# Kernel optimization log

Hardware: AMD Instinct MI355X
Metric: run time of the kernel (lower is better)

The kernel has to match this reference:

```python
import jax, jax.numpy as jnp
import numpy as np
import math

B, S, D, H = 2, 2048, 1024, 16
HD = D // H  # head dim = 64


def setup_inputs() -> dict:
    key = jax.random.key(0)
    k1, k2, k3, k4, k5 = jax.random.split(key, 5)
    query = jax.random.normal(k1, (B, S, D), dtype=jnp.float32)
    # tail padding: sequence lengths 1536 and 1792 -> positions >= length are padded (True)
    lengths = jnp.array([1536, 1792], dtype=jnp.int32)
    padding_mask = jnp.arange(S, dtype=jnp.int32)[None, :] >= lengths[:, None]  # [B,S] bool
    qkv_w = jax.random.normal(k2, (3 * D, D), dtype=jnp.float32) * 0.02
    qkv_b = jax.random.uniform(k3, (3 * D,), dtype=jnp.float32, minval=-0.03, maxval=0.03)
    out_w = jax.random.normal(k4, (D, D), dtype=jnp.float32) * 0.02
    out_b = jax.random.uniform(k5, (D,), dtype=jnp.float32, minval=-0.03, maxval=0.03)
    return {"query": query, "padding_mask": padding_mask,
            "qkv_w": qkv_w, "qkv_b": qkv_b, "out_w": out_w, "out_b": out_b}


def reference(query, padding_mask, qkv_w, qkv_b, out_w, out_b):
    # self-attention path (qkv_same=True): fused qkv projection then split
    qkv = query @ qkv_w.T + qkv_b                      # [B,S,3D]
    q, k, v = jnp.split(qkv, 3, axis=-1)               # each [B,S,D]

    def split_heads(x):
        return x.reshape(B, S, H, HD).transpose(0, 2, 1, 3)  # [B,H,S,HD]

    q, k, v = split_heads(q), split_heads(k), split_heads(v)

    # scores scaled by sqrt(head_dim)
    w = jnp.einsum('bhqd,bhkd->bhqk', q, k) / math.sqrt(HD)  # [B,H,S,S]

    # causal (future) mask: strict upper triangle masked
    future = jnp.triu(jnp.ones((S, S), dtype=bool), 1)
    w = jnp.where(future[None, None, :, :], -jnp.inf, w)
    # key padding mask
    w = jnp.where(padding_mask[:, None, None, :], -jnp.inf, w)

    a = jax.nn.softmax(w, axis=-1)
    # rows of fully-padded sequences are zeroed (dropout is identity in eval)
    all_masked = jnp.all(padding_mask, axis=-1)        # [B]
    a = jnp.where(all_masked[:, None, None, None], 0.0, a)

    x = jnp.einsum('bhqk,bhkd->bhqd', a, v)            # [B,H,S,HD]
    x = x.transpose(0, 2, 1, 3).reshape(B, S, D)       # merge heads
    return x @ out_w.T + out_b
```

## Files before the change

### kernel.cpp

```cpp
#include <hip/hip_runtime.h>
#include <hip/hip_bf16.h>
#include <stdint.h>

#define S_  2048
#define B_  2
#define H_  16
#define D_  1024
#define HD_ 64

typedef short short8 __attribute__((ext_vector_type(8)));
typedef float f32x4  __attribute__((ext_vector_type(4)));
typedef float f32x16 __attribute__((ext_vector_type(16)));

__device__ __forceinline__ unsigned short bf16_rne(float f) {
  unsigned int u = __float_as_uint(f);
  u += 0x7fffu + ((u >> 16) & 1u);
  return (unsigned short)(u >> 16);
}

__device__ __forceinline__ f32x4 mfma_bf16(short8 a, short8 b, f32x4 c) {
  return __builtin_amdgcn_mfma_f32_16x16x32_bf16(a, b, c, 0, 0, 0);
}

__device__ __forceinline__ f32x16 mfma32(short8 a, short8 b, f32x16 c) {
  return __builtin_amdgcn_mfma_f32_32x32x16_bf16(a, b, c, 0, 0, 0);
}

__device__ __forceinline__ unsigned int cvtpk_bf16(float lo, float hi) {
  unsigned int r;
  asm("v_cvt_pk_bf16_f32 %0, %1, %2" : "=v"(r) : "v"(lo), "v"(hi));
  return r;
}

__global__ void cvt3_kernel(const float* __restrict__ a, unsigned short* __restrict__ oa, int na8,
                            const float* __restrict__ b, unsigned short* __restrict__ ob, int nb8,
                            const float* __restrict__ c, unsigned short* __restrict__ oc, int nc8) {
  int i = blockIdx.x * blockDim.x + threadIdx.x;
  const float* in; unsigned short* out; int idx;
  if (i < na8) { in = a; out = oa; idx = i; }
  else if (i < na8 + nb8) { in = b; out = ob; idx = i - na8; }
  else if (i < na8 + nb8 + nc8) { in = c; out = oc; idx = i - na8 - nb8; }
  else return;
  const float4* p = (const float4*)in + (size_t)idx * 2;
  float4 x = p[0], y = p[1];
  union { unsigned short u[8]; short8 v; } r;
  r.u[0] = bf16_rne(x.x); r.u[1] = bf16_rne(x.y);
  r.u[2] = bf16_rne(x.z); r.u[3] = bf16_rne(x.w);
  r.u[4] = bf16_rne(y.x); r.u[5] = bf16_rne(y.y);
  r.u[6] = bf16_rne(y.z); r.u[7] = bf16_rne(y.w);
  *((short8*)out + idx) = r.v;
}

__global__ void lengths_kernel(const void* __restrict__ mask, int* __restrict__ lens) {
  __shared__ int mn[B_];
  __shared__ int anyb;
  int t = threadIdx.x;
  if (t < B_) mn[t] = S_;
  if (t == 0) anyb = 0;
  __syncthreads();
  const unsigned char* mb = (const unsigned char*)mask;
  for (int i = t; i < B_ * S_; i += 256) {
    if (mb[i]) { anyb = 1; atomicMin(&mn[i >> 11], i & (S_ - 1)); }
  }
  __syncthreads();
  if (!anyb) {
    const int* mi = (const int*)mask;
    for (int i = t; i < B_ * S_; i += 256) {
      if (mi[i]) atomicMin(&mn[i >> 11], i & (S_ - 1));
    }
    __syncthreads();
  }
  if (t < B_) lens[t] = mn[t];
}

__global__ __launch_bounds__(512, 2) void gemm8p_kernel(
    const unsigned short* __restrict__ A,
    const unsigned short* __restrict__ W,
    int K, int NBX,
    const float* __restrict__ bias,
    unsigned short* __restrict__ qb,
    unsigned short* __restrict__ kb,
    unsigned short* __restrict__ vb) {
  __shared__ __align__(16) unsigned short lds[65536];

  const int nwg = gridDim.x;
  const int cpx = nwg >> 3;
  const int bid = blockIdx.x;
  const int virt = (bid & 7) * cpx + (bid >> 3);
  const int bx = virt % NBX, by = virt / NBX;
  const int tile_m = by * 256, tile_n = bx * 256;
  const int t = threadIdx.x;
  const int lane = t & 63, w = t >> 6;
  const int wm = w >> 2, wn = w & 3;
  const int l15 = lane & 15, lk = lane >> 4;
  const int NT = K >> 6;

  f32x4 acc[8][4];
#pragma unroll
  for (int i = 0; i < 8; i++)
#pragma unroll
    for (int j = 0; j < 4; j++) { f32x4 z = {0.f, 0.f, 0.f, 0.f}; acc[i][j] = z; }

  const int L0 = t, L1 = 512 + t;
  const int r0 = L0 >> 3, c0 = (L0 & 7) ^ (r0 & 7);
  const int r1 = L1 >> 3, c1 = (L1 & 7) ^ (r1 & 7);

#define STAGE_HALF(SRC, GROW0, DSTE, KC)                                      \
  {                                                                           \
    __builtin_amdgcn_global_load_lds(                                         \
        (const __attribute__((address_space(1))) void*)(                      \
            (SRC) + (size_t)((GROW0) + r0) * K + (KC) + c0 * 8),              \
        (__attribute__((address_space(3))) void*)(&lds[(DSTE) + L0 * 8]),     \
        16, 0, 0);                                                            \
    __builtin_amdgcn_global_load_lds(                                         \
        (const __attribute__((address_space(1))) void*)(                      \
            (SRC) + (size_t)((GROW0) + r1) * K + (KC) + c1 * 8),              \
        (__attribute__((address_space(3))) void*)(&lds[(DSTE) + L1 * 8]),     \
        16, 0, 0);                                                            \
  }

  STAGE_HALF(A, tile_m,        0,    0);
  STAGE_HALF(W, tile_n,        32768, 0);
  STAGE_HALF(A, tile_m + 128,  8192, 0);
  STAGE_HALF(W, tile_n + 128,  32768 + 8192, 0);
  asm volatile("s_waitcnt vmcnt(4)" ::: "memory");
  __builtin_amdgcn_s_barrier();

  for (int tc = 0; tc < NT; ++tc) {
    const int cb = (tc & 1) * 16384;
    const int ob = ((tc & 1) ^ 1) * 16384;
    int tn = tc + 1; if (tn >= NT) tn = NT - 1;
    const int k0n = tn << 6;

#pragma unroll
    for (int p = 0; p < 4; ++p) {
      const int mh = (p & 1);
      const int nh = (p >> 1);
      short8 af[4][2], bfr[2][2];
#pragma unroll
      for (int fi = 0; fi < 4; ++fi) {
        const int rl = fi * 32 + wm * 16 + l15;
#pragma unroll
        for (int ks = 0; ks < 2; ++ks) {
          const int sw = (ks * 4 + lk) ^ (rl & 7);
          af[fi][ks] = *(const short8*)&lds[cb + mh * 8192 + rl * 64 + sw * 8];
        }
      }
#pragma unroll
      for (int fj = 0; fj < 2; ++fj) {
        const int cl = wn * 32 + fj * 16 + l15;
#pragma unroll
        for (int ks = 0; ks < 2; ++ks) {
          const int sw = (ks * 4 + lk) ^ (cl & 7);
          bfr[fj][ks] =
              *(const short8*)&lds[32768 + cb + nh * 8192 + cl * 64 + sw * 8];
        }
      }
      if (p == 0)      STAGE_HALF(A, tile_m,       ob,                k0n)
      else if (p == 1) STAGE_HALF(W, tile_n,       32768 + ob,        k0n)
      else if (p == 2) STAGE_HALF(A, tile_m + 128, ob + 8192,         k0n)
      else             STAGE_HALF(W, tile_n + 128, 32768 + ob + 8192, k0n);
      if (p != 2) asm volatile("s_waitcnt vmcnt(4)" ::: "memory");
      else        asm volatile("" ::: "memory");
      __builtin_amdgcn_s_barrier();
      asm volatile("s_waitcnt lgkmcnt(0)" ::: "memory");
      __builtin_amdgcn_s_setprio(1);
#pragma unroll
      for (int fi = 0; fi < 4; ++fi)
#pragma unroll
        for (int fj = 0; fj < 2; ++fj)
#pragma unroll
          for (int ks = 0; ks < 2; ++ks)
            acc[mh * 4 + fi][nh * 2 + fj] =
                mfma_bf16(af[fi][ks], bfr[fj][ks], acc[mh * 4 + fi][nh * 2 + fj]);
      __builtin_amdgcn_s_setprio(0);
      __builtin_amdgcn_s_barrier();
    }
  }
  asm volatile("s_waitcnt vmcnt(0)" ::: "memory");
#undef STAGE_HALF

#pragma unroll
  for (int j = 0; j < 4; ++j) {
    const int gn = tile_n + (j >> 1) * 128 + wn * 32 + (j & 1) * 16 + l15;
    const float bv = bias[gn];
    const int which = gn >> 10, dd = gn & (D_ - 1);
    const int h = dd >> 6, d = dd & 63;
    unsigned short* dstp = (which == 0) ? qb : (which == 1) ? kb : vb;
    const float mul = (which == 0) ? 0.125f : 1.0f;
#pragma unroll
    for (int i = 0; i < 8; ++i) {
      const int gmb = tile_m + (i >> 2) * 128 + (i & 3) * 32 + wm * 16 + lk * 4;
#pragma unroll
      for (int r = 0; r < 4; ++r) {
        const int gm = gmb + r;
        const int bb = gm >> 11, s = gm & (S_ - 1);
        dstp[((size_t)((bb * H_ + h) * S_ + s)) * HD_ + d] =
            bf16_rne((acc[i][j][r] + bv) * mul);
      }
    }
  }
}

__global__ __launch_bounds__(256) void gemm_bt_kernel(
    const unsigned short* __restrict__ A,
    const unsigned short* __restrict__ W,
    int K, int N,
    const float* __restrict__ bias,
    float* __restrict__ outf) {
  __shared__ unsigned short As[128 * 32];
  __shared__ unsigned short Bs[128 * 32];
  const int tile_m = blockIdx.y * 128;
  const int tile_n = blockIdx.x * 128;
  const int t = threadIdx.x;
  const int lane = t & 63;
  const int w = t >> 6;
  const int wr = w >> 1, wc = w & 1;
  const int l15 = lane & 15, lk = lane >> 4;

  f32x4 acc[4][4];
#pragma unroll
  for (int i = 0; i < 4; i++)
#pragma unroll
    for (int j = 0; j < 4; j++) { f32x4 z = {0.f, 0.f, 0.f, 0.f}; acc[i][j] = z; }

  for (int k0 = 0; k0 < K; k0 += 32) {
#pragma unroll
    for (int c = 0; c < 2; ++c) {
      int e = (c * 256 + t) * 8;
      int row = e >> 5, col = e & 31;
      __builtin_amdgcn_global_load_lds(
          (__attribute__((address_space(1))) void*)(A + (size_t)(tile_m + row) * K + k0 + col),
          (__attribute__((address_space(3))) void*)(&As[e]), 16, 0, 0);
      __builtin_amdgcn_global_load_lds(
          (__attribute__((address_space(1))) void*)(W + (size_t)(tile_n + row) * K + k0 + col),
          (__attribute__((address_space(3))) void*)(&Bs[e]), 16, 0, 0);
    }
    asm volatile("s_waitcnt vmcnt(0)" ::: "memory");
    __syncthreads();

    short8 af[4], bfr[4];
#pragma unroll
    for (int i = 0; i < 4; i++)
      af[i] = *(const short8*)&As[(wr * 64 + i * 16 + l15) * 32 + lk * 8];
#pragma unroll
    for (int j = 0; j < 4; j++)
      bfr[j] = *(const short8*)&Bs[(wc * 64 + j * 16 + l15) * 32 + lk * 8];
#pragma unroll
    for (int i = 0; i < 4; i++)
#pragma unroll
      for (int j = 0; j < 4; j++)
        acc[i][j] = mfma_bf16(af[i], bfr[j], acc[i][j]);
    __syncthreads();
  }

#pragma unroll
  for (int i = 0; i < 4; i++) {
#pragma unroll
    for (int j = 0; j < 4; j++) {
      int gn = tile_n + wc * 64 + j * 16 + l15;
      float bv = bias[gn];
#pragma unroll
      for (int r = 0; r < 4; r++) {
        int gm = tile_m + wr * 64 + i * 16 + lk * 4 + r;
        outf[(size_t)gm * N + gn] = acc[i][j][r] + bv;
      }
    }
  }
}

__global__ __launch_bounds__(256, 3) void attn_kernel(
    const unsigned short* __restrict__ qbuf,
    const unsigned short* __restrict__ kbuf,
    const unsigned short* __restrict__ vbuf,
    const int* __restrict__ lens,
    unsigned short* __restrict__ attn_out) {
  __shared__ __align__(16) char smem[33792];
  __shared__ float lsh[2][64];

  const int bid = blockIdx.x;
  const int xcd = bid & 7, nn = bid >> 3;
  const int rr = nn >> 5, cc = nn & 31;
  const int bh = (xcd << 2) | (cc & 3);
  const int qlo = cc >> 2;
  const int qt = (rr & 1) ? (8 * rr + 7 - qlo) : (8 * rr + qlo);
  const int b = bh >> 4;
  const int len = lens[b];
  const int t = threadIdx.x;
  const int lane = t & 63, w = t >> 6;
  const int g = w >> 1, wq = w & 1;
  const int l31 = lane & 31, hi = lane >> 5;
  const int hi8 = hi * 8, hi4 = hi * 4;
  const int q0 = qt * 64 + wq * 32;
  const int qme = q0 + l31;

  unsigned short* Ks = (unsigned short*)(smem + g * 8192);
  unsigned int*   Vt = (unsigned int*)(smem + 16384 + g * 8704);

  const unsigned short* qbh = qbuf + (size_t)bh * S_ * HD_;
  const unsigned short* kbh = kbuf + (size_t)bh * S_ * HD_;
  const unsigned short* vbh = vbuf + (size_t)bh * S_ * HD_;

  short8 qf[4];
#pragma unroll
  for (int ds = 0; ds < 4; ++ds)
    qf[ds] = *(const short8*)&qbh[(size_t)(q0 + l31) * HD_ + ds * 16 + hi8];

  f32x16 o[2] = {{}, {}};
  float rsum = 0.f;

  const int ke = (len - 1) >> 6;
  const int kt_end = qt < ke ? qt : ke;
  const int NI = (kt_end >> 1) + 1;

  const int tg = t & 127;
  const int kr0 = tg >> 3, kc0 = tg & 7;
  const int vr2 = tg & 31, vcb = (tg >> 5) << 1;

  short8 pk[4], pva0 = {}, pva1 = {}, pvb0 = {}, pvb1 = {};
#pragma unroll
  for (int m = 0; m < 4; ++m) pk[m] = pva0;

#define LDG(KT)                                                               \
  {                                                                           \
    int ks_ = (KT) * 64;                                                      \
    pk[0] = *(const short8*)&kbh[(size_t)(ks_ + kr0     ) * HD_ + kc0 * 8];   \
    pk[1] = *(const short8*)&kbh[(size_t)(ks_ + kr0 + 16) * HD_ + kc0 * 8];   \
    pk[2] = *(const short8*)&kbh[(size_t)(ks_ + kr0 + 32) * HD_ + kc0 * 8];   \
    pk[3] = *(const short8*)&kbh[(size_t)(ks_ + kr0 + 48) * HD_ + kc0 * 8];   \
    const unsigned short* vp = vbh + (size_t)(ks_ + 2 * vr2) * HD_ + vcb * 8; \
    pva0 = *(const short8*)vp;       pva1 = *(const short8*)(vp + HD_);       \
    pvb0 = *(const short8*)(vp + 8); pvb1 = *(const short8*)(vp + HD_ + 8);   \
  }

  int my_kt = g;
  bool act = (my_kt <= kt_end);
  if (act) LDG(my_kt);

  typedef union { unsigned int u[4]; short8 s; } pa_t;

  for (int i = 0; i < NI; ++i) {
    __syncthreads();
    if (act) {
#pragma unroll
      for (int m = 0; m < 4; ++m) {
        const int r = kr0 + 16 * m;
        *(short8*)&Ks[r * 64 + ((kc0 ^ (r & 7)) << 3)] = pk[m];
      }
#pragma unroll
      for (int j = 0; j < 8; ++j) {
        unsigned int w0 = (unsigned int)(unsigned short)pva0[j] |
                          ((unsigned int)(unsigned short)pva1[j] << 16);
        unsigned int w1 = (unsigned int)(unsigned short)pvb0[j] |
                          ((unsigned int)(unsigned short)pvb1[j] << 16);
        Vt[(vcb * 8 + j) * 34 + vr2] = w0;
        Vt[((vcb + 1) * 8 + j) * 34 + vr2] = w1;
      }
    }
    __syncthreads();
    const int nxt = my_kt + 2;
    const bool nact = (nxt <= kt_end);
    if (nact) LDG(nxt);

    const int ks0 = my_kt * 64;
    if (act && ks0 <= q0 + 31) {
      const bool needM = (ks0 + 63 >= q0) || (ks0 + 63 >= len);
      const bool dokb1 = (ks0 + 32 <= q0 + 31) && (ks0 + 32 < len);

      pa_t pa[4];
      {
        f32x16 s0 = {};
#pragma unroll
        for (int ds = 0; ds < 4; ++ds) {
          const int cg = ((ds << 1) | hi) ^ (l31 & 7);
          const short8 kf = *(const short8*)&Ks[l31 * 64 + (cg << 3)];
          s0 = mfma32(kf, qf[ds], s0);
        }
        float pr[16];
#pragma unroll
        for (int r = 0; r < 16; ++r) {
          const int crow = (r & 3) + 8 * (r >> 2) + hi4;
          float p = __expf(s0[r]);
          if (needM) {
            const int key = ks0 + crow;
            if (key > qme || key >= len) p = 0.f;
          }
          pr[r] = p; rsum += p;
        }
        unsigned int A0 = cvtpk_bf16(pr[0], pr[1]);
        unsigned int A1 = cvtpk_bf16(pr[2], pr[3]);
        unsigned int B0 = cvtpk_bf16(pr[4], pr[5]);
        unsigned int B1 = cvtpk_bf16(pr[6], pr[7]);
        asm volatile("v_permlane32_swap_b32 %0, %1" : "+v"(A0), "+v"(B0));
        asm volatile("v_permlane32_swap_b32 %0, %1" : "+v"(A1), "+v"(B1));
        pa[0].u[0] = A0; pa[0].u[1] = A1; pa[0].u[2] = B0; pa[0].u[3] = B1;
        unsigned int C0 = cvtpk_bf16(pr[8], pr[9]);
        unsigned int C1 = cvtpk_bf16(pr[10], pr[11]);
        unsigned int D0 = cvtpk_bf16(pr[12], pr[13]);
        unsigned int D1 = cvtpk_bf16(pr[14], pr[15]);
        asm volatile("v_permlane32_swap_b32 %0, %1" : "+v"(C0), "+v"(D0));
        asm volatile("v_permlane32_swap_b32 %0, %1" : "+v"(C1), "+v"(D1));
        pa[1].u[0] = C0; pa[1].u[1] = C1; pa[1].u[2] = D0; pa[1].u[3] = D1;
      }
      if (dokb1) {
        f32x16 s1 = {};
#pragma unroll
        for (int ds = 0; ds < 4; ++ds) {
          const int cg = ((ds << 1) | hi) ^ (l31 & 7);
          const short8 kf = *(const short8*)&Ks[(32 + l31) * 64 + (cg << 3)];
          s1 = mfma32(kf, qf[ds], s1);
        }
        float pr[16];
#pragma unroll
        for (int r = 0; r < 16; ++r) {
          const int crow = 32 + (r & 3) + 8 * (r >> 2) + hi4;
          float p = __expf(s1[r]);
          if (needM) {
            const int key = ks0 + crow;
            if (key > qme || key >= len) p = 0.f;
          }
          pr[r] = p; rsum += p;
        }
        unsigned int A0 = cvtpk_bf16(pr[0], pr[1]);
        unsigned int A1 = cvtpk_bf16(pr[2], pr[3]);
        unsigned int B0 = cvtpk_bf16(pr[4], pr[5]);
        unsigned int B1 = cvtpk_bf16(pr[6], pr[7]);
        asm volatile("v_permlane32_swap_b32 %0, %1" : "+v"(A0), "+v"(B0));
        asm volatile("v_permlane32_swap_b32 %0, %1" : "+v"(A1), "+v"(B1));
        pa[2].u[0] = A0; pa[2].u[1] = A1; pa[2].u[2] = B0; pa[2].u[3] = B1;
        unsigned int C0 = cvtpk_bf16(pr[8], pr[9]);
        unsigned int C1 = cvtpk_bf16(pr[10], pr[11]);
        unsigned int D0 = cvtpk_bf16(pr[12], pr[13]);
        unsigned int D1 = cvtpk_bf16(pr[14], pr[15]);
        asm volatile("v_permlane32_swap_b32 %0, %1" : "+v"(C0), "+v"(D0));
        asm volatile("v_permlane32_swap_b32 %0, %1" : "+v"(C1), "+v"(D1));
        pa[3].u[0] = C0; pa[3].u[1] = C1; pa[3].u[2] = D0; pa[3].u[3] = D1;
      }
#pragma unroll
      for (int dh = 0; dh < 2; ++dh) {
        const int vbase = (dh * 32 + l31) * 34 + hi4;
#pragma unroll
        for (int ks = 0; ks < 4; ++ks) {
          if (ks >= 2 && !dokb1) continue;
          uint2 va = *(const uint2*)&Vt[vbase + 8 * ks];
          uint2 vb2 = *(const uint2*)&Vt[vbase + 8 * ks + 2];
          pa_t vv;
          vv.u[0] = va.x; vv.u[1] = va.y; vv.u[2] = vb2.x; vv.u[3] = vb2.y;
          o[dh] = mfma32(pa[ks].s, vv.s, o[dh]);
        }
      }
    }
    my_kt = nxt; act = nact;
  }
#undef LDG

  rsum += __shfl_xor(rsum, 32, 64);

  float* mo = (float*)smem;
  __syncthreads();
  if (g == 1) {
#pragma unroll
    for (int r = 0; r < 16; ++r) {
      const int qb = wq * 32 + (r & 3) + 8 * (r >> 2) + hi4;
      mo[qb * 66 + l31]      = o[0][r];
      mo[qb * 66 + 32 + l31] = o[1][r];
    }
    if (hi == 0) lsh[1][wq * 32 + l31] = rsum;
  }
  __syncthreads();
  if (g == 0) {
    const float lt = rsum + lsh[1][wq * 32 + l31];
    const float inv = (lt > 0.f) ? (1.0f / lt) : 0.f;
    if (hi == 0) lsh[0][wq * 32 + l31] = inv;
#pragma unroll
    for (int r = 0; r < 16; ++r) {
      const int cr = (r & 3) + 8 * (r >> 2) + hi4;
      const int qb = wq * 32 + cr;
      const float iv = lsh[0][wq * 32 + cr];
      const int s = qt * 64 + qb;
      unsigned short* op =
          &attn_out[((size_t)(b * S_ + s)) * D_ + (bh & 15) * HD_ + l31];
      op[0]  = bf16_rne((o[0][r] + mo[qb * 66 + l31]) * iv);
      op[32] = bf16_rne((o[1][r] + mo[qb * 66 + 32 + l31]) * iv);
    }
  }
}

extern "C" void kernel_launch(void* const* d_in, const int* in_sizes, int n_in,
                              void* d_out, int out_size, void* d_ws, size_t ws_size,
                              hipStream_t stream) {
  const float* query = (const float*)d_in[0];
  const void*  mask  = d_in[1];
  const float* qkv_w = (const float*)d_in[2];
  const float* qkv_b = (const float*)d_in[3];
  const float* out_w = (const float*)d_in[4];
  const float* out_b = (const float*)d_in[5];
  float* out = (float*)d_out;

  char* ws = (char*)d_ws;
  unsigned short* qx     = (unsigned short*)(ws);
  unsigned short* wqkv   = (unsigned short*)(ws + (8u  << 20));
  unsigned short* wout   = (unsigned short*)(ws + (14u << 20));
  unsigned short* qbuf   = (unsigned short*)(ws + (16u << 20));
  unsigned short* kbuf   = (unsigned short*)(ws + (24u << 20));
  unsigned short* vbuf   = (unsigned short*)(ws + (32u << 20));
  unsigned short* attn_o = qx;
  int* lens              = (int*)(ws + (40u << 20));

  lengths_kernel<<<1, 256, 0, stream>>>(mask, lens);
  const int na8 = B_ * S_ * D_ / 8, nb8 = 3 * D_ * D_ / 8, nc8 = D_ * D_ / 8;
  cvt3_kernel<<<(na8 + nb8 + nc8) / 256, 256, 0, stream>>>(
      query, qx, na8, qkv_w, wqkv, nb8, out_w, wout, nc8);

  gemm8p_kernel<<<192, 512, 0, stream>>>(qx, wqkv, D_, 3 * D_ / 256, qkv_b,
                                         qbuf, kbuf, vbuf);

  attn_kernel<<<1024, 256, 0, stream>>>(qbuf, kbuf, vbuf, lens, attn_o);

  dim3 g2(D_ / 128, B_ * S_ / 128);
  gemm_bt_kernel<<<g2, 256, 0, stream>>>(attn_o, wout, D_, D_, out_b, out);
}
```

Before: 136.5 us.

## Split attention key tiles across four warp groups and use exp2 with folded log2e

The attention block grows from 256 to 512 threads, so four warp groups each take every fourth key tile instead of two groups taking every other one. Shared memory doubles to hold the extra K/V staging, and the end-of-kernel reduction now sums three partial O tiles and row sums through LDS. Separately, log2(e) is folded into the Q scale in the QKV GEMM epilogue so the softmax can call exp2f instead of __expf. The aim is shorter serial key loops per block and cheaper exponentials, at the cost of a larger final reduction, more LDS per block and a different occupancy balance.

```diff
diff --git a/kernel.cpp b/kernel.cpp
--- a/kernel.cpp
+++ b/kernel.cpp
@@ -187,7 +187,7 @@
     const int which = gn >> 10, dd = gn & (D_ - 1);
     const int h = dd >> 6, d = dd & 63;
     unsigned short* dstp = (which == 0) ? qb : (which == 1) ? kb : vb;
-    const float mul = (which == 0) ? 0.125f : 1.0f;
+    const float mul = (which == 0) ? 0.18033688011112042f : 1.0f;
 #pragma unroll
     for (int i = 0; i < 8; ++i) {
       const int gmb = tile_m + (i >> 2) * 128 + (i & 3) * 32 + wm * 16 + lk * 4;
@@ -269,14 +269,15 @@
   }
 }
 
-__global__ __launch_bounds__(256, 3) void attn_kernel(
+__global__ __launch_bounds__(512, 2) void attn_kernel(
     const unsigned short* __restrict__ qbuf,
     const unsigned short* __restrict__ kbuf,
     const unsigned short* __restrict__ vbuf,
     const int* __restrict__ lens,
     unsigned short* __restrict__ attn_out) {
-  __shared__ __align__(16) char smem[33792];
-  __shared__ float lsh[2][64];
+  __shared__ __align__(16) char smem[67584];
+  __shared__ float pl[3][64];
+  __shared__ float lsh0[64];
 
   const int bid = blockIdx.x;
   const int xcd = bid & 7, nn = bid >> 3;
@@ -295,7 +296,7 @@
   const int qme = q0 + l31;
 
   unsigned short* Ks = (unsigned short*)(smem + g * 8192);
-  unsigned int*   Vt = (unsigned int*)(smem + 16384 + g * 8704);
+  unsigned int*   Vt = (unsigned int*)(smem + 32768 + g * 8704);
 
   const unsigned short* qbh = qbuf + (size_t)bh * S_ * HD_;
   const unsigned short* kbh = kbuf + (size_t)bh * S_ * HD_;
@@ -311,7 +312,7 @@
 
   const int ke = (len - 1) >> 6;
   const int kt_end = qt < ke ? qt : ke;
-  const int NI = (kt_end >> 1) + 1;
+  const int NI = (kt_end >> 2) + 1;
 
   const int tg = t & 127;
   const int kr0 = tg >> 3, kc0 = tg & 7;
@@ -358,7 +359,7 @@
       }
     }
     __syncthreads();
-    const int nxt = my_kt + 2;
+    const int nxt = my_kt + 4;
     const bool nact = (nxt <= kt_end);
     if (nact) LDG(nxt);
 
@@ -380,7 +381,7 @@
 #pragma unroll
         for (int r = 0; r < 16; ++r) {
           const int crow = (r & 3) + 8 * (r >> 2) + hi4;
-          float p = __expf(s0[r]);
+          float p = exp2f(s0[r]);
           if (needM) {
             const int key = ks0 + crow;
             if (key > qme || key >= len) p = 0.f;
@@ -414,7 +415,7 @@
 #pragma unroll
         for (int r = 0; r < 16; ++r) {
           const int crow = 32 + (r & 3) + 8 * (r >> 2) + hi4;
-          float p = __expf(s1[r]);
+          float p = exp2f(s1[r]);
           if (needM) {
             const int key = ks0 + crow;
             if (key > qme || key >= len) p = 0.f;
@@ -456,32 +457,39 @@
 
   rsum += __shfl_xor(rsum, 32, 64);
 
-  float* mo = (float*)smem;
+  float* po = (float*)smem;
   __syncthreads();
-  if (g == 1) {
+  if (g >= 1) {
+    float* pw = po + (g - 1) * 4224;
 #pragma unroll
     for (int r = 0; r < 16; ++r) {
       const int qb = wq * 32 + (r & 3) + 8 * (r >> 2) + hi4;
-      mo[qb * 66 + l31]      = o[0][r];
-      mo[qb * 66 + 32 + l31] = o[1][r];
-    }
-    if (hi == 0) lsh[1][wq * 32 + l31] = rsum;
+      pw[qb * 66 + l31]      = o[0][r];
+      pw[qb * 66 + 32 + l31] = o[1][r];
+    }
+    if (hi == 0) pl[g - 1][wq * 32 + l31] = rsum;
   }
   __syncthreads();
   if (g == 0) {
-    const float lt = rsum + lsh[1][wq * 32 + l31];
+    const int myrow = wq * 32 + l31;
+    const float lt = rsum + pl[0][myrow] + pl[1][myrow] + pl[2][myrow];
     const float inv = (lt > 0.f) ? (1.0f / lt) : 0.f;
-    if (hi == 0) lsh[0][wq * 32 + l31] = inv;
+    if (hi == 0) lsh0[myrow] = inv;
 #pragma unroll
     for (int r = 0; r < 16; ++r) {
       const int cr = (r & 3) + 8 * (r >> 2) + hi4;
       const int qb = wq * 32 + cr;
-      const float iv = lsh[0][wq * 32 + cr];
+      const float iv = lsh0[qb];
       const int s = qt * 64 + qb;
+      float o0 = o[0][r] + po[qb * 66 + l31] + po[4224 + qb * 66 + l31] +
+                 po[8448 + qb * 66 + l31];
+      float o1 = o[1][r] + po[qb * 66 + 32 + l31] +
+                 po[4224 + qb * 66 + 32 + l31] +
+                 po[8448 + qb * 66 + 32 + l31];
       unsigned short* op =
           &attn_out[((size_t)(b * S_ + s)) * D_ + (bh & 15) * HD_ + l31];
-      op[0]  = bf16_rne((o[0][r] + mo[qb * 66 + l31]) * iv);
-      op[32] = bf16_rne((o[1][r] + mo[qb * 66 + 32 + l31]) * iv);
+      op[0]  = bf16_rne(o0 * iv);
+      op[32] = bf16_rne(o1 * iv);
     }
   }
 }
@@ -515,7 +523,7 @@
   gemm8p_kernel<<<192, 512, 0, stream>>>(qx, wqkv, D_, 3 * D_ / 256, qkv_b,
                                          qbuf, kbuf, vbuf);
 
-  attn_kernel<<<1024, 256, 0, stream>>>(qbuf, kbuf, vbuf, lens, attn_o);
+  attn_kernel<<<1024, 512, 0, stream>>>(qbuf, kbuf, vbuf, lens, attn_o);
 
   dim3 g2(D_ / 128, B_ * S_ / 128);
   gemm_bt_kernel<<<g2, 256, 0, stream>>>(attn_o, wout, D_, D_, out_b, out);
```

After: 157.6 us. +15.4%, slower.

## Emit V transposed from QKV GEMM and read it directly in attention

Applied to the files above, without the earlier changes.

The QKV projection epilogue now writes V in a head-dim-major [B,H,HD,S] layout, so the attention kernel loads PV MFMA operands straight from global memory instead of staging and transposing V through LDS. This removes the V LDS writes and reads and halves attention shared memory, which may raise occupancy. It also folds log2(e) into the Q scale so softmax uses exp2f instead of __expf. The cost is uncoalesced V reads from global/L2 inside the inner loop and scattered 8-byte stores in the GEMM epilogue.

```diff
diff --git a/kernel.cpp b/kernel.cpp
--- a/kernel.cpp
+++ b/kernel.cpp
@@ -80,7 +80,7 @@
     const float* __restrict__ bias,
     unsigned short* __restrict__ qb,
     unsigned short* __restrict__ kb,
-    unsigned short* __restrict__ vb) {
+    unsigned short* __restrict__ vt) {
   __shared__ __align__(16) unsigned short lds[65536];
 
   const int nwg = gridDim.x;
@@ -186,17 +186,23 @@
     const float bv = bias[gn];
     const int which = gn >> 10, dd = gn & (D_ - 1);
     const int h = dd >> 6, d = dd & 63;
-    unsigned short* dstp = (which == 0) ? qb : (which == 1) ? kb : vb;
-    const float mul = (which == 0) ? 0.125f : 1.0f;
+    const float mul = (which == 0) ? 0.18033688011112042f : 1.0f;
 #pragma unroll
     for (int i = 0; i < 8; ++i) {
       const int gmb = tile_m + (i >> 2) * 128 + (i & 3) * 32 + wm * 16 + lk * 4;
-#pragma unroll
-      for (int r = 0; r < 4; ++r) {
-        const int gm = gmb + r;
-        const int bb = gm >> 11, s = gm & (S_ - 1);
-        dstp[((size_t)((bb * H_ + h) * S_ + s)) * HD_ + d] =
-            bf16_rne((acc[i][j][r] + bv) * mul);
+      const int bb = gmb >> 11, s0v = gmb & (S_ - 1);
+      if (which == 2) {
+        union { unsigned short u[4]; uint2 v2; } pk4;
+#pragma unroll
+        for (int r = 0; r < 4; ++r) pk4.u[r] = bf16_rne(acc[i][j][r] + bv);
+        *(uint2*)&vt[((size_t)(bb * H_ + h) * HD_ + d) * S_ + s0v] = pk4.v2;
+      } else {
+        unsigned short* dstp = (which == 0) ? qb : kb;
+#pragma unroll
+        for (int r = 0; r < 4; ++r) {
+          dstp[((size_t)((bb * H_ + h) * S_ + s0v + r)) * HD_ + d] =
+              bf16_rne((acc[i][j][r] + bv) * mul);
+        }
       }
     }
   }
@@ -272,10 +278,10 @@
 __global__ __launch_bounds__(256, 3) void attn_kernel(
     const unsigned short* __restrict__ qbuf,
     const unsigned short* __restrict__ kbuf,
-    const unsigned short* __restrict__ vbuf,
+    const unsigned short* __restrict__ vtbuf,
     const int* __restrict__ lens,
     unsigned short* __restrict__ attn_out) {
-  __shared__ __align__(16) char smem[33792];
+  __shared__ __align__(16) char smem[16896];
   __shared__ float lsh[2][64];
 
   const int bid = blockIdx.x;
@@ -295,11 +301,10 @@
   const int qme = q0 + l31;
 
   unsigned short* Ks = (unsigned short*)(smem + g * 8192);
-  unsigned int*   Vt = (unsigned int*)(smem + 16384 + g * 8704);
 
   const unsigned short* qbh = qbuf + (size_t)bh * S_ * HD_;
   const unsigned short* kbh = kbuf + (size_t)bh * S_ * HD_;
-  const unsigned short* vbh = vbuf + (size_t)bh * S_ * HD_;
+  const unsigned short* vth = vtbuf + (size_t)bh * HD_ * S_;
 
   short8 qf[4];
 #pragma unroll
@@ -315,11 +320,8 @@
 
   const int tg = t & 127;
   const int kr0 = tg >> 3, kc0 = tg & 7;
-  const int vr2 = tg & 31, vcb = (tg >> 5) << 1;
-
-  short8 pk[4], pva0 = {}, pva1 = {}, pvb0 = {}, pvb1 = {};
-#pragma unroll
-  for (int m = 0; m < 4; ++m) pk[m] = pva0;
+
+  short8 pk[4] = {};
 
 #define LDG(KT)                                                               \
   {                                                                           \
@@ -328,9 +330,6 @@
     pk[1] = *(const short8*)&kbh[(size_t)(ks_ + kr0 + 16) * HD_ + kc0 * 8];   \
     pk[2] = *(const short8*)&kbh[(size_t)(ks_ + kr0 + 32) * HD_ + kc0 * 8];   \
     pk[3] = *(const short8*)&kbh[(size_t)(ks_ + kr0 + 48) * HD_ + kc0 * 8];   \
-    const unsigned short* vp = vbh + (size_t)(ks_ + 2 * vr2) * HD_ + vcb * 8; \
-    pva0 = *(const short8*)vp;       pva1 = *(const short8*)(vp + HD_);       \
-    pvb0 = *(const short8*)(vp + 8); pvb1 = *(const short8*)(vp + HD_ + 8);   \
   }
 
   int my_kt = g;
@@ -346,15 +345,6 @@
       for (int m = 0; m < 4; ++m) {
         const int r = kr0 + 16 * m;
         *(short8*)&Ks[r * 64 + ((kc0 ^ (r & 7)) << 3)] = pk[m];
-      }
-#pragma unroll
-      for (int j = 0; j < 8; ++j) {
-        unsigned int w0 = (unsigned int)(unsigned short)pva0[j] |
-                          ((unsigned int)(unsigned short)pva1[j] << 16);
-        unsigned int w1 = (unsigned int)(unsigned short)pvb0[j] |
-                          ((unsigned int)(unsigned short)pvb1[j] << 16);
-        Vt[(vcb * 8 + j) * 34 + vr2] = w0;
-        Vt[((vcb + 1) * 8 + j) * 34 + vr2] = w1;
       }
     }
     __syncthreads();
@@ -380,7 +370,7 @@
 #pragma unroll
         for (int r = 0; r < 16; ++r) {
           const int crow = (r & 3) + 8 * (r >> 2) + hi4;
-          float p = __expf(s0[r]);
+          float p = exp2f(s0[r]);
           if (needM) {
             const int key = ks0 + crow;
             if (key > qme || key >= len) p = 0.f;
@@ -414,7 +404,7 @@
 #pragma unroll
         for (int r = 0; r < 16; ++r) {
           const int crow = 32 + (r & 3) + 8 * (r >> 2) + hi4;
-          float p = __expf(s1[r]);
+          float p = exp2f(s1[r]);
           if (needM) {
             const int key = ks0 + crow;
             if (key > qme || key >= len) p = 0.f;
@@ -438,15 +428,13 @@
       }
 #pragma unroll
       for (int dh = 0; dh < 2; ++dh) {
-        const int vbase = (dh * 32 + l31) * 34 + hi4;
-#pragma unroll
-        for (int ks = 0; ks < 4; ++ks) {
-          if (ks >= 2 && !dokb1) continue;
-          uint2 va = *(const uint2*)&Vt[vbase + 8 * ks];
-          uint2 vb2 = *(const uint2*)&Vt[vbase + 8 * ks + 2];
-          pa_t vv;
-          vv.u[0] = va.x; vv.u[1] = va.y; vv.u[2] = vb2.x; vv.u[3] = vb2.y;
-          o[dh] = mfma32(pa[ks].s, vv.s, o[dh]);
+        const unsigned short* vrow =
+            &vth[(size_t)(dh * 32 + l31) * S_ + ks0 + hi8];
+#pragma unroll
+        for (int c = 0; c < 4; ++c) {
+          if (c >= 2 && !dokb1) continue;
+          const short8 vv = *(const short8*)&vrow[c * 16];
+          o[dh] = mfma32(pa[c].s, vv, o[dh]);
         }
       }
     }
@@ -503,7 +491,7 @@
   unsigned short* wout   = (unsigned short*)(ws + (14u << 20));
   unsigned short* qbuf   = (unsigned short*)(ws + (16u << 20));
   unsigned short* kbuf   = (unsigned short*)(ws + (24u << 20));
-  unsigned short* vbuf   = (unsigned short*)(ws + (32u << 20));
+  unsigned short* vtbuf  = (unsigned short*)(ws + (32u << 20));
   unsigned short* attn_o = qx;
   int* lens              = (int*)(ws + (40u << 20));
 
@@ -513,9 +501,9 @@
       query, qx, na8, qkv_w, wqkv, nb8, out_w, wout, nc8);
 
   gemm8p_kernel<<<192, 512, 0, stream>>>(qx, wqkv, D_, 3 * D_ / 256, qkv_b,
-                                         qbuf, kbuf, vbuf);
-
-  attn_kernel<<<1024, 256, 0, stream>>>(qbuf, kbuf, vbuf, lens, attn_o);
+                                         qbuf, kbuf, vtbuf);
+
+  attn_kernel<<<1024, 256, 0, stream>>>(qbuf, kbuf, vtbuf, lens, attn_o);
 
   dim3 g2(D_ / 128, B_ * S_ / 128);
   gemm_bt_kernel<<<g2, 256, 0, stream>>>(attn_o, wout, D_, D_, out_b, out);
```

After: 144.3 us. 5.7% more time.

## Widen attention blocks to 128 queries and fold log2e into Q scaling

Applied to the files above, without the earlier changes.

Each attention block now has 512 threads and covers 128 query rows instead of 64. Four query warps per group share each K/V tile staged in shared memory, which halves global K/V traffic and staging work per query. The grid shrinks to 512 blocks, with a new pairing of query tiles to keep causal work balanced. Separately, the Q scale now includes log2(e), so the softmax can use exp2f instead of __expf. The cost is fewer, larger blocks, possibly lower occupancy, and more idle warps on causal diagonal tiles.

```diff
diff --git a/kernel.cpp b/kernel.cpp
--- a/kernel.cpp
+++ b/kernel.cpp
@@ -187,7 +187,7 @@
     const int which = gn >> 10, dd = gn & (D_ - 1);
     const int h = dd >> 6, d = dd & 63;
     unsigned short* dstp = (which == 0) ? qb : (which == 1) ? kb : vb;
-    const float mul = (which == 0) ? 0.125f : 1.0f;
+    const float mul = (which == 0) ? 0.18033688011112042f : 1.0f;
 #pragma unroll
     for (int i = 0; i < 8; ++i) {
       const int gmb = tile_m + (i >> 2) * 128 + (i & 3) * 32 + wm * 16 + lk * 4;
@@ -269,29 +269,29 @@
   }
 }
 
-__global__ __launch_bounds__(256, 3) void attn_kernel(
+__global__ __launch_bounds__(512, 2) void attn_kernel(
     const unsigned short* __restrict__ qbuf,
     const unsigned short* __restrict__ kbuf,
     const unsigned short* __restrict__ vbuf,
     const int* __restrict__ lens,
     unsigned short* __restrict__ attn_out) {
   __shared__ __align__(16) char smem[33792];
-  __shared__ float lsh[2][64];
+  __shared__ float lsh[2][128];
 
   const int bid = blockIdx.x;
   const int xcd = bid & 7, nn = bid >> 3;
   const int rr = nn >> 5, cc = nn & 31;
   const int bh = (xcd << 2) | (cc & 3);
   const int qlo = cc >> 2;
-  const int qt = (rr & 1) ? (8 * rr + 7 - qlo) : (8 * rr + qlo);
+  const int qt2 = rr ? (15 - qlo) : qlo;
   const int b = bh >> 4;
   const int len = lens[b];
   const int t = threadIdx.x;
   const int lane = t & 63, w = t >> 6;
-  const int g = w >> 1, wq = w & 1;
+  const int g = w >> 2, wq = w & 3;
   const int l31 = lane & 31, hi = lane >> 5;
   const int hi8 = hi * 8, hi4 = hi * 4;
-  const int q0 = qt * 64 + wq * 32;
+  const int q0 = qt2 * 128 + wq * 32;
   const int qme = q0 + l31;
 
   unsigned short* Ks = (unsigned short*)(smem + g * 8192);
@@ -310,31 +310,28 @@
   float rsum = 0.f;
 
   const int ke = (len - 1) >> 6;
-  const int kt_end = qt < ke ? qt : ke;
-  const int NI = (kt_end >> 1) + 1;
-
-  const int tg = t & 127;
+  const int kt_eb0 = 2 * qt2 + 1;
+  const int kt_endb = kt_eb0 < ke ? kt_eb0 : ke;
+  const int NI = (kt_endb >> 1) + 1;
+
+  const int tg = t & 255;
   const int kr0 = tg >> 3, kc0 = tg & 7;
-  const int vr2 = tg & 31, vcb = (tg >> 5) << 1;
-
-  short8 pk[4], pva0 = {}, pva1 = {}, pvb0 = {}, pvb1 = {};
-#pragma unroll
-  for (int m = 0; m < 4; ++m) pk[m] = pva0;
+  const int vr2 = tg & 31, vcg = tg >> 5;
+
+  short8 pk0 = {}, pk1 = {}, pva0 = {}, pva1 = {};
 
 #define LDG(KT)                                                               \
   {                                                                           \
     int ks_ = (KT) * 64;                                                      \
-    pk[0] = *(const short8*)&kbh[(size_t)(ks_ + kr0     ) * HD_ + kc0 * 8];   \
-    pk[1] = *(const short8*)&kbh[(size_t)(ks_ + kr0 + 16) * HD_ + kc0 * 8];   \
-    pk[2] = *(const short8*)&kbh[(size_t)(ks_ + kr0 + 32) * HD_ + kc0 * 8];   \
-    pk[3] = *(const short8*)&kbh[(size_t)(ks_ + kr0 + 48) * HD_ + kc0 * 8];   \
-    const unsigned short* vp = vbh + (size_t)(ks_ + 2 * vr2) * HD_ + vcb * 8; \
-    pva0 = *(const short8*)vp;       pva1 = *(const short8*)(vp + HD_);       \
-    pvb0 = *(const short8*)(vp + 8); pvb1 = *(const short8*)(vp + HD_ + 8);   \
+    pk0 = *(const short8*)&kbh[(size_t)(ks_ + kr0     ) * HD_ + kc0 * 8];     \
+    pk1 = *(const short8*)&kbh[(size_t)(ks_ + kr0 + 32) * HD_ + kc0 * 8];     \
+    const unsigned short* vp = vbh + (size_t)(ks_ + 2 * vr2) * HD_ + vcg * 8; \
+    pva0 = *(const short8*)vp;                                                \
+    pva1 = *(const short8*)(vp + HD_);                                        \
   }
 
   int my_kt = g;
-  bool act = (my_kt <= kt_end);
+  bool act = (my_kt <= kt_endb);
   if (act) LDG(my_kt);
 
   typedef union { unsigned int u[4]; short8 s; } pa_t;
@@ -342,24 +339,20 @@
   for (int i = 0; i < NI; ++i) {
     __syncthreads();
     if (act) {
-#pragma unroll
-      for (int m = 0; m < 4; ++m) {
-        const int r = kr0 + 16 * m;
-        *(short8*)&Ks[r * 64 + ((kc0 ^ (r & 7)) << 3)] = pk[m];
-      }
+      *(short8*)&Ks[kr0 * 64 + ((kc0 ^ (kr0 & 7)) << 3)] = pk0;
+      const int r1 = kr0 + 32;
+      *(short8*)&Ks[r1 * 64 + ((kc0 ^ (r1 & 7)) << 3)] = pk1;
 #pragma unroll
       for (int j = 0; j < 8; ++j) {
+        const int d = vcg * 8 + j;
         unsigned int w0 = (unsigned int)(unsigned short)pva0[j] |
                           ((unsigned int)(unsigned short)pva1[j] << 16);
-        unsigned int w1 = (unsigned int)(unsigned short)pvb0[j] |
-                          ((unsigned int)(unsigned short)pvb1[j] << 16);
-        Vt[(vcb * 8 + j) * 34 + vr2] = w0;
-        Vt[((vcb + 1) * 8 + j) * 34 + vr2] = w1;
+        Vt[d * 34 + vr2] = w0;
       }
     }
     __syncthreads();
     const int nxt = my_kt + 2;
-    const bool nact = (nxt <= kt_end);
+    const bool nact = (nxt <= kt_endb);
     if (nact) LDG(nxt);
 
     const int ks0 = my_kt * 64;
@@ -380,7 +373,7 @@
 #pragma unroll
         for (int r = 0; r < 16; ++r) {
           const int crow = (r & 3) + 8 * (r >> 2) + hi4;
-          float p = __expf(s0[r]);
+          float p = exp2f(s0[r]);
           if (needM) {
             const int key = ks0 + crow;
             if (key > qme || key >= len) p = 0.f;
@@ -414,7 +407,7 @@
 #pragma unroll
         for (int r = 0; r < 16; ++r) {
           const int crow = 32 + (r & 3) + 8 * (r >> 2) + hi4;
-          float p = __expf(s1[r]);
+          float p = exp2f(s1[r]);
           if (needM) {
             const int key = ks0 + crow;
             if (key > qme || key >= len) p = 0.f;
@@ -476,8 +469,8 @@
     for (int r = 0; r < 16; ++r) {
       const int cr = (r & 3) + 8 * (r >> 2) + hi4;
       const int qb = wq * 32 + cr;
-      const float iv = lsh[0][wq * 32 + cr];
-      const int s = qt * 64 + qb;
+      const float iv = lsh[0][qb];
+      const int s = qt2 * 128 + qb;
       unsigned short* op =
           &attn_out[((size_t)(b * S_ + s)) * D_ + (bh & 15) * HD_ + l31];
       op[0]  = bf16_rne((o[0][r] + mo[qb * 66 + l31]) * iv);
@@ -515,7 +508,7 @@
   gemm8p_kernel<<<192, 512, 0, stream>>>(qx, wqkv, D_, 3 * D_ / 256, qkv_b,
                                          qbuf, kbuf, vbuf);
 
-  attn_kernel<<<1024, 256, 0, stream>>>(qbuf, kbuf, vbuf, lens, attn_o);
+  attn_kernel<<<512, 512, 0, stream>>>(qbuf, kbuf, vbuf, lens, attn_o);
 
   dim3 g2(D_ / 128, B_ * S_ / 128);
   gemm_bt_kernel<<<g2, 256, 0, stream>>>(attn_o, wout, D_, D_, out_b, out);
```

Measured after the change: 137.9 us. Within noise of the previous version (+1.0%).
